# Kernel optimization log

Measured on AMD Instinct MI355X. Metric: run time of the kernel, lower is better.

## Reference

```python
import jax, jax.numpy as jnp
import numpy as np

IN_UNITS = 128
N_DRUG, N_DIS, N_EDGE = 10000, 5000, 2000000


def setup_inputs() -> dict:
    key = jax.random.key(0)
    ks = jax.random.split(key, 10)
    s1 = 1.0 / np.sqrt(2 * IN_UNITS)
    s2 = 1.0 / np.sqrt(128)
    s3 = 1.0 / np.sqrt(64)
    return {
        "drug_feat": jax.random.normal(ks[0], (N_DRUG, IN_UNITS), dtype=jnp.float32),
        "dis_feat": jax.random.normal(ks[1], (N_DIS, IN_UNITS), dtype=jnp.float32),
        "edge_index": jax.random.randint(ks[2], (2, N_EDGE), 0, N_DIS, dtype=jnp.int64),
        "W1": jax.random.uniform(ks[3], (128, 2 * IN_UNITS), jnp.float32, -s1, s1),
        "b1": jax.random.uniform(ks[4], (128,), jnp.float32, -s1, s1),
        "W2": jax.random.uniform(ks[5], (64, 128), jnp.float32, -s2, s2),
        "b2": jax.random.uniform(ks[6], (64,), jnp.float32, -s2, s2),
        "W3": jax.random.uniform(ks[7], (1, 64), jnp.float32, -s3, s3),
        "b3": jax.random.uniform(ks[8], (1,), jnp.float32, -s3, s3),
    }


def reference(drug_feat, dis_feat, edge_index, W1, b1, W2, b2, W3, b3):
    # Gather endpoint features and concat along feature dim: [E, 2*in_units]
    edge_feat = jnp.concatenate(
        (drug_feat[edge_index[0]], dis_feat[edge_index[1]]), axis=1
    )
    # 3-layer MLP (Dropout is identity in eval mode)
    h = jax.nn.relu(edge_feat @ W1.T + b1)  # [E, 128]
    h = jax.nn.relu(h @ W2.T + b2)          # [E, 64]
    return h @ W3.T + b3                     # [E, 1]
```

## Files before the change

kernel.cpp:

```cpp
#include <hip/hip_runtime.h>


typedef __bf16 bf16x8 __attribute__((ext_vector_type(8)));
typedef unsigned short u16x8 __attribute__((ext_vector_type(8)));
typedef float f32x4 __attribute__((ext_vector_type(4)));

static __device__ __forceinline__ unsigned short f2b(float f) {
  unsigned int u = __builtin_bit_cast(unsigned int, f);
  u += 0x7FFFu + ((u >> 16) & 1u);
  return (unsigned short)(u >> 16);
}

static __device__ __forceinline__ f32x4 mfma_bf16(u16x8 a, u16x8 b, f32x4 c) {
  return __builtin_amdgcn_mfma_f32_16x16x32_bf16(
      __builtin_bit_cast(bf16x8, a), __builtin_bit_cast(bf16x8, b), c, 0, 0, 0);
}

__global__ void cvt_tables(const float* __restrict__ a, const float* __restrict__ b,
                           unsigned short* __restrict__ oa, unsigned short* __restrict__ ob,
                           int na, int nb) {
  const int t = blockIdx.x * blockDim.x + threadIdx.x;
  const int ta = na >> 3;
  const float* src;
  unsigned short* dst;
  int i;
  if (t < ta) {
    src = a; dst = oa; i = t;
  } else {
    i = t - ta;
    if (i >= (nb >> 3)) return;
    src = b; dst = ob;
  }
  const float4 f0 = *(const float4*)(src + i * 8);
  const float4 f1 = *(const float4*)(src + i * 8 + 4);
  u16x8 v;
  v[0] = f2b(f0.x); v[1] = f2b(f0.y); v[2] = f2b(f0.z); v[3] = f2b(f0.w);
  v[4] = f2b(f1.x); v[5] = f2b(f1.y); v[6] = f2b(f1.z); v[7] = f2b(f1.w);
  *(u16x8*)(dst + i * 8) = v;
}

__global__ void cvt_weights(const float* __restrict__ W1, const float* __restrict__ W2,
                            unsigned short* __restrict__ o1, unsigned short* __restrict__ o2) {
  const int t = blockIdx.x * blockDim.x + threadIdx.x;
  if (t < 4096) {
    const int l = t & 63, kt = (t >> 6) & 7, ut = t >> 9;
    const int n = 16 * ut + (l & 15), k0 = 32 * kt + 8 * (l >> 4);
    const float* src = W1 + n * 256 + k0;
    u16x8 v;
#pragma unroll
    for (int j = 0; j < 8; ++j) v[j] = f2b(src[j]);
    *(u16x8*)(o1 + t * 8) = v;
  } else if (t < 5120) {
    const int u = t - 4096;
    const int l = u & 63, kt = (u >> 6) & 3, nt = u >> 8;
    const int n = 16 * nt + (l & 15), k0 = 32 * kt + 8 * (l >> 4);
    const float* src = W2 + n * 128 + k0;
    u16x8 v;
#pragma unroll
    for (int j = 0; j < 8; ++j) v[j] = f2b(src[j]);
    *(u16x8*)(o2 + u * 8) = v;
  }
}

__global__ __launch_bounds__(256, 4) void mlp_fused(
    const unsigned short* __restrict__ drugB, const unsigned short* __restrict__ disB,
    const int* __restrict__ eidx, const unsigned short* __restrict__ w1frag,
    const unsigned short* __restrict__ w2frag, const float* __restrict__ b1,
    const float* __restrict__ b2, const float* __restrict__ W3,
    const float* __restrict__ b3, float* __restrict__ out, int E) {
  __shared__ __align__(16) unsigned char smem[32768];
  unsigned char* Abase = smem;

  const int tid = threadIdx.x;
  const int wn = tid >> 6;
  const int l = tid & 63;
  const int l15 = l & 15;
  const int lq = l >> 4;
  const int e0 = blockIdx.x * 64;

  {
    const int q = wn;
    int e = e0 + l;
    if (e >= E) e = E - 1;
    const int idx = eidx[(q >> 1) * E + e];
    const unsigned short* src = ((q < 2) ? drugB : disB) + (long)idx * 128 + (q & 1) * 64;
    unsigned char* rowp = Abase + l * 512;
    const int base = q * 128;
    const int swz = (l & 7) << 4;
#pragma unroll
    for (int c = 0; c < 8; ++c) {
      const u16x8 v = *(const u16x8*)(src + c * 8);
      *(u16x8*)(rowp + ((base + c * 16) ^ swz)) = v;
    }
  }

  const float4 b1v0 = *(const float4*)(b1 + 32 * wn + 4 * lq);
  const float4 b1v1 = *(const float4*)(b1 + 32 * wn + 16 + 4 * lq);
  __syncthreads();

  f32x4 acc1[2][4];
#pragma unroll
  for (int uti = 0; uti < 2; ++uti)
#pragma unroll
    for (int nt = 0; nt < 4; ++nt) acc1[uti][nt] = (f32x4){0.f, 0.f, 0.f, 0.f};

  const unsigned short* w1p = w1frag + ((2 * wn) * 512 + l) * 8;
  u16x8 nf[2][2];
  nf[0][0] = *(const u16x8*)(w1p);
  nf[0][1] = *(const u16x8*)(w1p + 512 * 8);
  nf[1][0] = *(const u16x8*)(w1p + 64 * 8);
  nf[1][1] = *(const u16x8*)(w1p + (512 + 64) * 8);
#pragma unroll
  for (int kt = 0; kt < 8; ++kt) {
    const u16x8 c0 = nf[kt & 1][0], c1 = nf[kt & 1][1];
    if (kt < 6) {
      nf[kt & 1][0] = *(const u16x8*)(w1p + ((kt + 2) * 64) * 8);
      nf[kt & 1][1] = *(const u16x8*)(w1p + ((512 + (kt + 2) * 64)) * 8);
    }
#pragma unroll
    for (int nt = 0; nt < 4; ++nt) {
      const int e = 16 * nt + l15;
      const u16x8 b = *(const u16x8*)(Abase + e * 512 + ((64 * kt + 16 * lq) ^ ((e & 7) << 4)));
      acc1[0][nt] = mfma_bf16(c0, b, acc1[0][nt]);
      acc1[1][nt] = mfma_bf16(c1, b, acc1[1][nt]);
    }
  }
  __syncthreads();

#pragma unroll
  for (int uti = 0; uti < 2; ++uti) {
    const float4 bv = uti ? b1v1 : b1v0;
#pragma unroll
    for (int nt = 0; nt < 4; ++nt) {
      const int e = 16 * nt + l15;
      float h0 = acc1[uti][nt][0] + bv.x; h0 = h0 > 0.f ? h0 : 0.f;
      float h1 = acc1[uti][nt][1] + bv.y; h1 = h1 > 0.f ? h1 : 0.f;
      float h2 = acc1[uti][nt][2] + bv.z; h2 = h2 > 0.f ? h2 : 0.f;
      float h3 = acc1[uti][nt][3] + bv.w; h3 = h3 > 0.f ? h3 : 0.f;
      ushort4 hv;
      hv.x = f2b(h0); hv.y = f2b(h1); hv.z = f2b(h2); hv.w = f2b(h3);
      *(ushort4*)(Abase + e * 256 + ((64 * wn + 32 * uti + 8 * lq) ^ ((e & 7) << 4))) = hv;
    }
  }
  __syncthreads();

  const int e = 16 * wn + l15;
  f32x4 acc2[4];
#pragma unroll
  for (int nt = 0; nt < 4; ++nt) acc2[nt] = (f32x4){0.f, 0.f, 0.f, 0.f};
#pragma unroll
  for (int kt = 0; kt < 4; ++kt) {
    const u16x8 b = *(const u16x8*)(Abase + e * 256 + ((64 * kt + 16 * lq) ^ ((e & 7) << 4)));
#pragma unroll
    for (int nt = 0; nt < 4; ++nt) {
      const u16x8 a = *(const u16x8*)(w2frag + ((nt * 4 + kt) * 64 + l) * 8);
      acc2[nt] = mfma_bf16(a, b, acc2[nt]);
    }
  }

  float s = 0.f;
#pragma unroll
  for (int nt = 0; nt < 4; ++nt) {
    const float4 b2v = *(const float4*)(b2 + 16 * nt + 4 * lq);
    const float4 w3v = *(const float4*)(W3 + 16 * nt + 4 * lq);
    float h;
    h = acc2[nt][0] + b2v.x; s += (h > 0.f ? h : 0.f) * w3v.x;
    h = acc2[nt][1] + b2v.y; s += (h > 0.f ? h : 0.f) * w3v.y;
    h = acc2[nt][2] + b2v.z; s += (h > 0.f ? h : 0.f) * w3v.z;
    h = acc2[nt][3] + b2v.w; s += (h > 0.f ? h : 0.f) * w3v.w;
  }
  s += __shfl_xor(s, 16, 64);
  s += __shfl_xor(s, 32, 64);
  if (l < 16) {
    const int eo = e0 + 16 * wn + l15;
    if (eo < E) out[eo] = s + b3[0];
  }
}

extern "C" void kernel_launch(void* const* d_in, const int* in_sizes, int n_in,
                              void* d_out, int out_size, void* d_ws, size_t ws_size,
                              hipStream_t stream) {
  const float* drug = (const float*)d_in[0];
  const float* dis = (const float*)d_in[1];
  const int* eidx = (const int*)d_in[2];
  const float* W1 = (const float*)d_in[3];
  const float* b1 = (const float*)d_in[4];
  const float* W2 = (const float*)d_in[5];
  const float* b2 = (const float*)d_in[6];
  const float* W3 = (const float*)d_in[7];
  const float* b3 = (const float*)d_in[8];
  float* out = (float*)d_out;

  const int na = in_sizes[0];
  const int nb = in_sizes[1];
  const int E = in_sizes[2] / 2;

  unsigned short* ws = (unsigned short*)d_ws;
  unsigned short* drugB = ws;
  unsigned short* disB = ws + na;
  unsigned short* w1f = ws + na + nb;
  unsigned short* w2f = w1f + 128 * 256;

  const int tct = (na + nb) >> 3;
  cvt_tables<<<(tct + 255) / 256, 256, 0, stream>>>(drug, dis, drugB, disB, na, nb);
  cvt_weights<<<20, 256, 0, stream>>>(W1, W2, w1f, w2f);

  const int grid = (E + 63) / 64;
  mlp_fused<<<grid, 256, 0, stream>>>(drugB, disB, eidx, w1f, w2f, b1, b2, W3, b3, out, E);
}
```

Measured before the change: 277.5 us.

## Make each wave own 32 edges, loading gathered features directly into MFMA operands

Each wave now processes its own 32 edges end to end. Gathered drug and disease rows go straight from global memory into MFMA B-fragments instead of being staged through shared memory, and the block-wide __syncthreads barriers are removed. Each wave computes all 128 hidden units, so W1 fragments are reloaded per wave from global/L2 rather than split across waves. The layer-1 output is kept in a per-wave LDS slice for layer 2. Block size grows to 128 edges, trading more accumulator registers and more weight traffic for no inter-wave synchronization and no LDS staging of inputs.

Result: slower. 371.4 us (+33.8%).

```diff
diff --git a/kernel.cpp b/kernel.cpp
--- a/kernel.cpp
+++ b/kernel.cpp
@@ -11,7 +11,7 @@
   return (unsigned short)(u >> 16);
 }
 
-static __device__ __forceinline__ f32x4 mfma_bf16(u16x8 a, u16x8 b, f32x4 c) {
+static __device__ __forceinline__ f32x4 mfma16(u16x8 a, u16x8 b, f32x4 c) {
   return __builtin_amdgcn_mfma_f32_16x16x32_bf16(
       __builtin_bit_cast(bf16x8, a), __builtin_bit_cast(bf16x8, b), c, 0, 0, 0);
 }
@@ -69,111 +69,96 @@
     const float* __restrict__ b2, const float* __restrict__ W3,
     const float* __restrict__ b3, float* __restrict__ out, int E) {
   __shared__ __align__(16) unsigned char smem[32768];
-  unsigned char* Abase = smem;
 
   const int tid = threadIdx.x;
-  const int wn = tid >> 6;
+  const int wv = tid >> 6;
   const int l = tid & 63;
   const int l15 = l & 15;
   const int lq = l >> 4;
-  const int e0 = blockIdx.x * 64;
+  const int e0w = blockIdx.x * 128 + wv * 32;
+  unsigned char* hb = smem + wv * 8192;
 
-  {
-    const int q = wn;
-    int e = e0 + l;
-    if (e >= E) e = E - 1;
-    const int idx = eidx[(q >> 1) * E + e];
-    const unsigned short* src = ((q < 2) ? drugB : disB) + (long)idx * 128 + (q & 1) * 64;
-    unsigned char* rowp = Abase + l * 512;
-    const int base = q * 128;
-    const int swz = (l & 7) << 4;
+  int eA = e0w + l15;      if (eA >= E) eA = E - 1;
+  int eB = e0w + 16 + l15; if (eB >= E) eB = E - 1;
+  const unsigned short* pd0 = drugB + (long)eidx[eA] * 128;
+  const unsigned short* pd1 = drugB + (long)eidx[eB] * 128;
+  const unsigned short* ps0 = disB + (long)eidx[E + eA] * 128;
+  const unsigned short* ps1 = disB + (long)eidx[E + eB] * 128;
+
+  f32x4 acc1[8][2];
 #pragma unroll
-    for (int c = 0; c < 8; ++c) {
-      const u16x8 v = *(const u16x8*)(src + c * 8);
-      *(u16x8*)(rowp + ((base + c * 16) ^ swz)) = v;
+  for (int ut = 0; ut < 8; ++ut) {
+    acc1[ut][0] = (f32x4){0.f, 0.f, 0.f, 0.f};
+    acc1[ut][1] = (f32x4){0.f, 0.f, 0.f, 0.f};
+  }
+  const unsigned short* w1l = w1frag + l * 8;
+#pragma unroll
+  for (int kt = 0; kt < 8; ++kt) {
+    const int fo = (kt & 3) * 32 + lq * 8;
+    const u16x8 b0 = *(const u16x8*)(((kt < 4) ? pd0 : ps0) + fo);
+    const u16x8 b1f = *(const u16x8*)(((kt < 4) ? pd1 : ps1) + fo);
+#pragma unroll
+    for (int ut = 0; ut < 8; ++ut) {
+      const u16x8 wf = *(const u16x8*)(w1l + (ut * 8 + kt) * 512);
+      acc1[ut][0] = mfma16(wf, b0, acc1[ut][0]);
+      acc1[ut][1] = mfma16(wf, b1f, acc1[ut][1]);
     }
   }
 
-  const float4 b1v0 = *(const float4*)(b1 + 32 * wn + 4 * lq);
-  const float4 b1v1 = *(const float4*)(b1 + 32 * wn + 16 + 4 * lq);
-  __syncthreads();
-
-  f32x4 acc1[2][4];
 #pragma unroll
-  for (int uti = 0; uti < 2; ++uti)
+  for (int ut = 0; ut < 8; ++ut) {
+    const float4 bv = *(const float4*)(b1 + 16 * ut + 4 * lq);
 #pragma unroll
-    for (int nt = 0; nt < 4; ++nt) acc1[uti][nt] = (f32x4){0.f, 0.f, 0.f, 0.f};
-
-  const unsigned short* w1p = w1frag + ((2 * wn) * 512 + l) * 8;
-  u16x8 nf[2][2];
-  nf[0][0] = *(const u16x8*)(w1p);
-  nf[0][1] = *(const u16x8*)(w1p + 512 * 8);
-  nf[1][0] = *(const u16x8*)(w1p + 64 * 8);
-  nf[1][1] = *(const u16x8*)(w1p + (512 + 64) * 8);
-#pragma unroll
-  for (int kt = 0; kt < 8; ++kt) {
-    const u16x8 c0 = nf[kt & 1][0], c1 = nf[kt & 1][1];
-    if (kt < 6) {
-      nf[kt & 1][0] = *(const u16x8*)(w1p + ((kt + 2) * 64) * 8);
-      nf[kt & 1][1] = *(const u16x8*)(w1p + ((512 + (kt + 2) * 64)) * 8);
-    }
-#pragma unroll
-    for (int nt = 0; nt < 4; ++nt) {
-      const int e = 16 * nt + l15;
-      const u16x8 b = *(const u16x8*)(Abase + e * 512 + ((64 * kt + 16 * lq) ^ ((e & 7) << 4)));
-      acc1[0][nt] = mfma_bf16(c0, b, acc1[0][nt]);
-      acc1[1][nt] = mfma_bf16(c1, b, acc1[1][nt]);
-    }
-  }
-  __syncthreads();
-
-#pragma unroll
-  for (int uti = 0; uti < 2; ++uti) {
-    const float4 bv = uti ? b1v1 : b1v0;
-#pragma unroll
-    for (int nt = 0; nt < 4; ++nt) {
-      const int e = 16 * nt + l15;
-      float h0 = acc1[uti][nt][0] + bv.x; h0 = h0 > 0.f ? h0 : 0.f;
-      float h1 = acc1[uti][nt][1] + bv.y; h1 = h1 > 0.f ? h1 : 0.f;
-      float h2 = acc1[uti][nt][2] + bv.z; h2 = h2 > 0.f ? h2 : 0.f;
-      float h3 = acc1[uti][nt][3] + bv.w; h3 = h3 > 0.f ? h3 : 0.f;
+    for (int nt = 0; nt < 2; ++nt) {
+      float h0 = acc1[ut][nt][0] + bv.x; h0 = h0 > 0.f ? h0 : 0.f;
+      float h1 = acc1[ut][nt][1] + bv.y; h1 = h1 > 0.f ? h1 : 0.f;
+      float h2 = acc1[ut][nt][2] + bv.z; h2 = h2 > 0.f ? h2 : 0.f;
+      float h3 = acc1[ut][nt][3] + bv.w; h3 = h3 > 0.f ? h3 : 0.f;
       ushort4 hv;
       hv.x = f2b(h0); hv.y = f2b(h1); hv.z = f2b(h2); hv.w = f2b(h3);
-      *(ushort4*)(Abase + e * 256 + ((64 * wn + 32 * uti + 8 * lq) ^ ((e & 7) << 4))) = hv;
-    }
-  }
-  __syncthreads();
-
-  const int e = 16 * wn + l15;
-  f32x4 acc2[4];
-#pragma unroll
-  for (int nt = 0; nt < 4; ++nt) acc2[nt] = (f32x4){0.f, 0.f, 0.f, 0.f};
-#pragma unroll
-  for (int kt = 0; kt < 4; ++kt) {
-    const u16x8 b = *(const u16x8*)(Abase + e * 256 + ((64 * kt + 16 * lq) ^ ((e & 7) << 4)));
-#pragma unroll
-    for (int nt = 0; nt < 4; ++nt) {
-      const u16x8 a = *(const u16x8*)(w2frag + ((nt * 4 + kt) * 64 + l) * 8);
-      acc2[nt] = mfma_bf16(a, b, acc2[nt]);
+      *(ushort4*)(hb + (2 * ut + (lq >> 1)) * 512 + (16 * nt + l15) * 16 + (lq & 1) * 8) = hv;
     }
   }
 
-  float s = 0.f;
+  f32x4 acc2[4][2];
 #pragma unroll
-  for (int nt = 0; nt < 4; ++nt) {
-    const float4 b2v = *(const float4*)(b2 + 16 * nt + 4 * lq);
-    const float4 w3v = *(const float4*)(W3 + 16 * nt + 4 * lq);
-    float h;
-    h = acc2[nt][0] + b2v.x; s += (h > 0.f ? h : 0.f) * w3v.x;
-    h = acc2[nt][1] + b2v.y; s += (h > 0.f ? h : 0.f) * w3v.y;
-    h = acc2[nt][2] + b2v.z; s += (h > 0.f ? h : 0.f) * w3v.z;
-    h = acc2[nt][3] + b2v.w; s += (h > 0.f ? h : 0.f) * w3v.w;
+  for (int nt2 = 0; nt2 < 4; ++nt2) {
+    acc2[nt2][0] = (f32x4){0.f, 0.f, 0.f, 0.f};
+    acc2[nt2][1] = (f32x4){0.f, 0.f, 0.f, 0.f};
   }
-  s += __shfl_xor(s, 16, 64);
-  s += __shfl_xor(s, 32, 64);
-  if (l < 16) {
-    const int eo = e0 + 16 * wn + l15;
-    if (eo < E) out[eo] = s + b3[0];
+  const unsigned short* w2l = w2frag + l * 8;
+#pragma unroll
+  for (int kt = 0; kt < 4; ++kt) {
+    const u16x8 h0 = *(const u16x8*)(hb + (4 * kt + lq) * 512 + l15 * 16);
+    const u16x8 h1 = *(const u16x8*)(hb + (4 * kt + lq) * 512 + (16 + l15) * 16);
+#pragma unroll
+    for (int nt2 = 0; nt2 < 4; ++nt2) {
+      const u16x8 wf = *(const u16x8*)(w2l + (nt2 * 4 + kt) * 512);
+      acc2[nt2][0] = mfma16(wf, h0, acc2[nt2][0]);
+      acc2[nt2][1] = mfma16(wf, h1, acc2[nt2][1]);
+    }
+  }
+
+  const float b3v = b3[0];
+#pragma unroll
+  for (int nt = 0; nt < 2; ++nt) {
+    float s = 0.f;
+#pragma unroll
+    for (int nt2 = 0; nt2 < 4; ++nt2) {
+      const float4 b2v = *(const float4*)(b2 + 16 * nt2 + 4 * lq);
+      const float4 w3v = *(const float4*)(W3 + 16 * nt2 + 4 * lq);
+      float h;
+      h = acc2[nt2][nt][0] + b2v.x; s += (h > 0.f ? h : 0.f) * w3v.x;
+      h = acc2[nt2][nt][1] + b2v.y; s += (h > 0.f ? h : 0.f) * w3v.y;
+      h = acc2[nt2][nt][2] + b2v.z; s += (h > 0.f ? h : 0.f) * w3v.z;
+      h = acc2[nt2][nt][3] + b2v.w; s += (h > 0.f ? h : 0.f) * w3v.w;
+    }
+    s += __shfl_xor(s, 16, 64);
+    s += __shfl_xor(s, 32, 64);
+    if (l < 16) {
+      const int e = e0w + 16 * nt + l15;
+      if (e < E) out[e] = s + b3v;
+    }
   }
 }
 
@@ -205,6 +190,6 @@
   cvt_tables<<<(tct + 255) / 256, 256, 0, stream>>>(drug, dis, drugB, disB, na, nb);
   cvt_weights<<<20, 256, 0, stream>>>(W1, W2, w1f, w2f);
 
-  const int grid = (E + 63) / 64;
+  const int grid = (E + 127) / 128;
   mlp_fused<<<grid, 256, 0, stream>>>(drugB, disB, eidx, w1f, w2f, b1, b2, W3, b3, out, E);
 }
```
